# Kernel tuning notes

Measured on AMD Instinct MI355X. Metric: run time of the kernel, lower is better.

The kernel has to match this reference:

```python
import jax, jax.numpy as jnp
import numpy as np

B, N, DM, DE, H, L = 4, 256, 128, 8, 2 and 2, 8  # placeholder, real values below
B, N, DM, DE, H, L = 4, 256, 128, 8, 8, 2
D = DM // H  # per-head dim = 16
INNER = H * D


def setup_inputs() -> dict:
    key = jax.random.key(0)
    ks = jax.random.split(key, 20)
    nodes = jax.random.normal(ks[0], (B, N, DM), dtype=jnp.float32)
    edges = jax.random.normal(ks[1], (B, N, N, DE), dtype=jnp.float32)
    adjacency = (jax.random.uniform(ks[2], (B, N, N)) < 0.1).astype(jnp.float32)
    s = 0.02
    p = {
        'Wq': jax.random.normal(ks[3], (L, DM, INNER)) * s,
        'bq': jnp.zeros((L, INNER)),
        'Wk': jax.random.normal(ks[4], (L, DM, INNER)) * s,
        'bk': jnp.zeros((L, INNER)),
        'Wv': jax.random.normal(ks[5], (L, DM, INNER)) * s,
        'bv': jnp.zeros((L, INNER)),
        'We': jax.random.normal(ks[6], (L, DE, INNER)) * s,
        'be': jnp.zeros((L, INNER)),
        'Wres': jax.random.normal(ks[7], (L, DM, DM)) * s,
        'bres': jnp.zeros((L, DM)),
        'Wgate': jax.random.normal(ks[8], (L, 3 * DM, 1)) * s,
        'ln_g': jnp.ones((L, DM)),
        'ln_b': jnp.zeros((L, DM)),
    }
    return {'nodes': nodes, 'edges': edges, 'adjacency': adjacency, **p}


def _adj_softmax(sim, adj):
    # Faithful to source: torch.mean(x, dim, keepdim=True)[0] indexes batch 0,
    # giving a (N,1) shift broadcast over all batch*head rows.
    means = jnp.mean(sim, axis=-1, keepdims=True)[0]
    x_exp = jnp.exp(sim - means) * adj
    s = jnp.sum(x_exp, axis=-1, keepdims=True)
    s = jnp.where(s == 0, 1.0, s)
    return x_exp / s


def reference(nodes, edges, adjacency, Wq, bq, Wk, bk, Wv, bv, We, be,
              Wres, bres, Wgate, ln_g, ln_b):
    b, n, dm = nodes.shape
    h, d = H, DM // H
    scale = 1.0 / jnp.sqrt(jnp.float32(d))
    adj = jnp.broadcast_to(adjacency[:, None], (b, h, n, n)).reshape(b * h, n, n)
    x = nodes
    for l in range(L):  # fixed small layer count
        def heads(t):  # (b,n,h*d) -> (b*h, n, d)
            return t.reshape(b, n, h, d).transpose(0, 2, 1, 3).reshape(b * h, n, d)
        q = heads(x @ Wq[l] + bq[l])
        k = heads(x @ Wk[l] + bk[l])
        v = heads(x @ Wv[l] + bv[l])
        # edge features: (b,n,n,h,d) -> (b*h, n, n, d)
        e = (edges @ We[l] + be[l]).reshape(b, n, n, h, d)
        e = e.transpose(0, 3, 1, 2, 4).reshape(b * h, n, n, d)
        ke = k[:, None, :, :] + e
        ve = v[:, None, :, :] + e
        sim = jnp.einsum('bid,bijd->bij', q, ke) * scale
        attn = _adj_softmax(sim, adj)
        out = jnp.einsum('bij,bijd->bid', attn, ve)
        out = out.reshape(b, h, n, d).transpose(0, 2, 1, 3).reshape(b, n, h * d)
        # GatedResidual
        res = x @ Wres[l] + bres[l]
        gate_in = jnp.concatenate([out, res, out - res], axis=-1)
        g = jax.nn.sigmoid(gate_in @ Wgate[l])
        y = out * g + res * (1 - g)
        mu = jnp.mean(y, axis=-1, keepdims=True)
        var = jnp.var(y, axis=-1, keepdims=True)
        y = (y - mu) / jnp.sqrt(var + 1e-5) * ln_g[l] + ln_b[l]
        x = jax.nn.relu(y)
    return x
```

## Files before the change

### kernel.cpp

```cpp
#include <hip/hip_runtime.h>

#define BB 4
#define NN 256
#define DMM 128
#define DEE 8
#define HH 8
#define DD 16
#define LAYERS 2
#define SCALE 0.25f
#define PS 260
#define SS (BB*NN*DMM)


struct Params {
  const float *nodes, *edges, *adjacency;
  const float *Wq, *bq, *Wk, *bk, *Wv, *bv, *We, *be, *Wres, *bres, *Wgate, *lng, *lnb;
  const float *src;
  float *q, *k, *v, *res;
  float *out;
  int layer;
};

__global__ __launch_bounds__(256) void k_proj(Params P){
  const int t = threadIdx.x;
  const int m = t >> 6;
  const int cp = t & 63;
  const int row0 = blockIdx.x * 2;
  const int l = P.layer;
  const float *W, *bia; float* dst;
  if (m==0){ W = P.Wq + l*DMM*DMM; bia = P.bq + l*DMM; dst = P.q; }
  else if (m==1){ W = P.Wk + l*DMM*DMM; bia = P.bk + l*DMM; dst = P.k; }
  else if (m==2){ W = P.Wv + l*DMM*DMM; bia = P.bv + l*DMM; dst = P.v; }
  else { W = P.Wres + l*DMM*DMM; bia = P.bres + l*DMM; dst = P.res; }
  const float2 bv2 = *(const float2*)(bia + 2*cp);
  float a00=bv2.x, a01=bv2.y, a10=bv2.x, a11=bv2.y;
  const float2* W2 = (const float2*)W;
  const float* xr = P.src + (size_t)row0*DMM;
  #pragma unroll 8
  for (int kk=0; kk<DMM; kk++){
    float2 w = W2[kk*64+cp];
    float x0 = xr[kk], x1 = xr[DMM+kk];
    a00 += x0*w.x; a01 += x0*w.y;
    a10 += x1*w.x; a11 += x1*w.y;
  }
  if (m==1){
    const int b = row0 >> 8, i0 = row0 & 255;
    float* kT = dst + ((size_t)b*DMM + 2*cp)*NN;
    kT[i0]      = a00;  kT[NN + i0]     = a01;
    kT[i0+1]    = a10;  kT[NN + i0+1]   = a11;
  } else {
    *(float2*)(dst + (size_t)row0*DMM     + 2*cp) = make_float2(a00,a01);
    *(float2*)(dst + (size_t)(row0+1)*DMM + 2*cp) = make_float2(a10,a11);
  }
}

__global__ __launch_bounds__(512) void k_mid(Params P){
  const int t = threadIdx.x;
  const int r = t >> 8;
  const int u = t & 255;
  const int row0 = blockIdx.x*2;
  const int row  = row0 + r;
  const int b = row0 >> 8;

  __shared__ float xloc[2][128];
  __shared__ float qs[2][128];
  __shared__ float res_s[2][128];
  __shared__ float qwe_s[2][64];
  __shared__ float qbe_s[2][8];
  __shared__ float es[2][8*PS];
  __shared__ float ps[2][8*PS];
  __shared__ float red_s[2][32];
  __shared__ float ssum_s[2][8];
  __shared__ float g_s[2][64];
  __shared__ float red_a[2][2], red_b[2][2], red_c[2][2];

  if (u < 128) qs[r][u]        = P.q  [(size_t)row*DMM + u];
  else         res_s[r][u-128] = P.res[(size_t)row*DMM + (u-128)];
  const int j = u;
  float ec[8]; float adj;
  {
    const float4* er4 = (const float4*)(P.edges + ((size_t)row*NN + j)*DEE);
    float4 e0 = er4[0], e1 = er4[1];
    ec[0]=e0.x; ec[1]=e0.y; ec[2]=e0.z; ec[3]=e0.w;
    ec[4]=e1.x; ec[5]=e1.y; ec[6]=e1.z; ec[7]=e1.w;
    #pragma unroll
    for (int c=0;c<8;c++) es[r][c*PS+j] = ec[c];
    adj = P.adjacency[(size_t)row*NN + j];
  }
  __syncthreads();

  if (u < 64){
    const int h = u>>3, c = u&7;
    const float* Wer = P.We + c*DMM + h*DD;
    float a = 0.f;
    #pragma unroll
    for (int d=0; d<DD; d++) a += qs[r][h*DD+d]*Wer[d];
    qwe_s[r][u] = a;
    if (c==0){
      const float* ber = P.be + h*DD;
      float a2=0.f;
      #pragma unroll
      for (int d=0; d<DD; d++) a2 += qs[r][h*DD+d]*ber[d];
      qbe_s[r][h] = a2;
    }
  }
  __syncthreads();

  {
    const float* kTj = P.k + (size_t)b*DMM*NN + j;
    float preg[8];
    #pragma unroll
    for (int h=0; h<HH; h++){
      const float* kc = kTj + (size_t)(h*DD)*NN;
      float sim = qbe_s[r][h];
      #pragma unroll
      for (int d=0; d<DD; d++) sim += qs[r][h*DD+d] * kc[(size_t)d*NN];
      const float4* qw4 = (const float4*)(&qwe_s[r][h*8]);
      float4 wA=qw4[0], wB=qw4[1];
      sim += ec[0]*wA.x + ec[1]*wA.y + ec[2]*wA.z + ec[3]*wA.w;
      sim += ec[4]*wB.x + ec[5]*wB.y + ec[6]*wB.z + ec[7]*wB.w;
      sim *= SCALE;
      float p = __expf(sim)*adj;
      preg[h]=p; ps[r][h*PS+j]=p;
    }
    #pragma unroll
    for (int h=0; h<HH; h++){
      float v = preg[h];
      #pragma unroll
      for (int off=32; off; off>>=1) v += __shfl_xor(v, off, 64);
      if ((u&63)==0) red_s[r][(u>>6)*8+h] = v;
    }
  }
  __syncthreads();

  float pv = 0.f;
  if (u < 128){
    const int h = u>>4;
    const float* vcol = P.v + (size_t)b*NN*DMM + u;
    const float4* pr = (const float4*)(&ps[r][h*PS]);
    #pragma unroll 4
    for (int jq=0; jq<64; jq++){
      float4 pp = pr[jq];
      const float* vv = vcol + jq*4*DMM;
      pv += pp.x*vv[0] + pp.y*vv[DMM] + pp.z*vv[2*DMM] + pp.w*vv[3*DMM];
    }
  } else if (u < 192){
    const int h=(u-128)>>3, c=(u-128)&7;
    const float4* pr = (const float4*)(&ps[r][h*PS]);
    const float4* er = (const float4*)(&es[r][c*PS]);
    float g=0.f;
    #pragma unroll 4
    for (int jq=0; jq<64; jq++){
      float4 pp=pr[jq], ee=er[jq];
      g += pp.x*ee.x + pp.y*ee.y + pp.z*ee.z + pp.w*ee.w;
    }
    g_s[r][h*8+c]=g;
  } else if (u >= 248){
    const int h=u-248;
    ssum_s[r][h] = red_s[r][h]+red_s[r][8+h]+red_s[r][16+h]+red_s[r][24+h];
  }
  __syncthreads();

  float o=0.f, rr=0.f;
  if (u<128){
    const int h = u>>4;
    const float* Wec = P.We + u;
    float eacc=0.f;
    #pragma unroll
    for (int c=0;c<8;c++) eacc += Wec[c*DMM]*g_s[r][h*8+c];
    const float ssum = ssum_s[r][h];
    const float denom = (ssum==0.f)?1.f:ssum;
    const float bev = P.be[u];
    o = (pv + eacc + ssum*bev)/denom;
    rr = res_s[r][u];
    const float* Wg = P.Wgate;
    float contrib = o*Wg[u] + rr*Wg[DMM+u] + (o-rr)*Wg[2*DMM+u];
    #pragma unroll
    for (int off=32; off; off>>=1) contrib += __shfl_xor(contrib, off, 64);
    if ((u&63)==0) red_a[r][u>>6]=contrib;
  }
  __syncthreads();

  float y=0.f;
  if (u<128){
    const float gs = red_a[r][0]+red_a[r][1];
    const float gate = 1.f/(1.f+__expf(-gs));
    y = o*gate + rr*(1.f-gate);
    float s1=y, s2=y*y;
    #pragma unroll
    for (int off=32; off; off>>=1){ s1+=__shfl_xor(s1,off,64); s2+=__shfl_xor(s2,off,64); }
    if ((u&63)==0){ red_b[r][u>>6]=s1; red_c[r][u>>6]=s2; }
  }
  __syncthreads();

  if (u<128){
    const float mu  = (red_b[r][0]+red_b[r][1])*(1.f/128.f);
    const float var = (red_c[r][0]+red_c[r][1])*(1.f/128.f) - mu*mu;
    const float inv = rsqrtf(var+1e-5f);
    float yn = (y-mu)*inv*P.lng[u] + P.lnb[u];
    xloc[r][u] = fmaxf(yn, 0.f);
  }
  __syncthreads();

  {
    const int w = t>>6, m = w&3, ri = w>>2, cp = t&63;
    const float *W, *bia; float* dst;
    if (m==0){ W=P.Wq+DMM*DMM;   bia=P.bq+DMM;   dst=P.q;   }
    else if (m==1){ W=P.Wk+DMM*DMM;   bia=P.bk+DMM;   dst=P.k;   }
    else if (m==2){ W=P.Wv+DMM*DMM;   bia=P.bv+DMM;   dst=P.v;   }
    else          { W=P.Wres+DMM*DMM; bia=P.bres+DMM; dst=P.res; }
    const float2 bv2 = *(const float2*)(bia+2*cp);
    float a0=bv2.x, a1=bv2.y;
    const float2* W2 = (const float2*)W;
    const float* xr = xloc[ri];
    #pragma unroll 8
    for (int kk=0; kk<DMM; kk++){
      float2 w2 = W2[kk*64+cp];
      float xv = xr[kk];
      a0 += xv*w2.x; a1 += xv*w2.y;
    }
    const int prow = row0 + ri;
    if (m==1){
      const int pb = prow >> 8, pi = prow & 255;
      float* kT = dst + SS + ((size_t)pb*DMM + 2*cp)*NN;
      kT[pi] = a0; kT[NN + pi] = a1;
    } else {
      *(float2*)(dst + SS + (size_t)prow*DMM + 2*cp) = make_float2(a0,a1);
    }
  }
}

__global__ __launch_bounds__(256) void k_attn(Params P){
  const int t = threadIdx.x;
  const int b = blockIdx.x >> 8;
  const int i = blockIdx.x & 255;
  const int l = P.layer;

  __shared__ float qs[128];
  __shared__ float qwe_s[64];
  __shared__ float qbe_s[8];
  __shared__ float es[8*PS];
  __shared__ float ps[8*PS];
  __shared__ float red_s[32];
  __shared__ float ssum_s[8];
  __shared__ float g_s[64];
  __shared__ float res_s[128];
  __shared__ float red_a[2], red_b[2], red_c[2];

  if (t < 128) qs[t] = P.q[(b*NN+i)*DMM + t];
  __syncthreads();
  if (t < 64){
    const int h = t>>3, c = t&7;
    const float* Wer = P.We + l*DEE*DMM + c*DMM + h*DD;
    float a = 0.f;
    #pragma unroll
    for (int d=0; d<DD; d++) a += qs[h*DD+d]*Wer[d];
    qwe_s[t] = a;
    if (c==0){
      const float* ber = P.be + l*DMM + h*DD;
      float a2 = 0.f;
      #pragma unroll
      for (int d=0; d<DD; d++) a2 += qs[h*DD+d]*ber[d];
      qbe_s[h] = a2;
    }
  }
  __syncthreads();

  {
    const int j = t;
    const float4* er4 = (const float4*)(P.edges + ((size_t)(b*NN+i)*NN + j)*DEE);
    float4 e0 = er4[0], e1 = er4[1];
    float ec[8] = {e0.x,e0.y,e0.z,e0.w, e1.x,e1.y,e1.z,e1.w};
    #pragma unroll
    for (int c=0;c<8;c++) es[c*PS+j] = ec[c];
    const float adj = P.adjacency[(size_t)(b*NN+i)*NN + j];
    const float* kTj = P.k + (size_t)b*DMM*NN + j;
    float preg[8];
    #pragma unroll
    for (int h=0; h<HH; h++){
      const float* kc = kTj + (size_t)(h*DD)*NN;
      float sim = qbe_s[h];
      #pragma unroll
      for (int d=0; d<DD; d++) sim += qs[h*DD+d] * kc[(size_t)d*NN];
      const float4* qw4 = (const float4*)(qwe_s + h*8);
      float4 wA = qw4[0], wB = qw4[1];
      sim += ec[0]*wA.x + ec[1]*wA.y + ec[2]*wA.z + ec[3]*wA.w;
      sim += ec[4]*wB.x + ec[5]*wB.y + ec[6]*wB.z + ec[7]*wB.w;
      sim *= SCALE;
      float p = __expf(sim) * adj;
      preg[h] = p;
      ps[h*PS+j] = p;
    }
    #pragma unroll
    for (int h=0; h<HH; h++){
      float v = preg[h];
      #pragma unroll
      for (int off=32; off; off>>=1) v += __shfl_xor(v, off, 64);
      if ((t&63)==0) red_s[(t>>6)*8 + h] = v;
    }
  }
  __syncthreads();

  float pv = 0.f;
  if (t < 128){
    const int h = t>>4;
    const float* vcol = P.v + b*NN*DMM + t;
    const float4* pr = (const float4*)(ps + h*PS);
    #pragma unroll 4
    for (int jq=0; jq<64; jq++){
      float4 pp = pr[jq];
      const float* vv = vcol + jq*4*DMM;
      pv += pp.x*vv[0] + pp.y*vv[DMM] + pp.z*vv[2*DMM] + pp.w*vv[3*DMM];
    }
  } else if (t < 192){
    const int h = (t-128)>>3, c = (t-128)&7;
    const float4* pr = (const float4*)(ps + h*PS);
    const float4* er = (const float4*)(es + c*PS);
    float g = 0.f;
    #pragma unroll 4
    for (int jq=0; jq<64; jq++){
      float4 pp = pr[jq], ee = er[jq];
      g += pp.x*ee.x + pp.y*ee.y + pp.z*ee.z + pp.w*ee.w;
    }
    g_s[h*8+c] = g;
  } else {
    const int u = t - 192;
    const float2 rv = *(const float2*)(P.res + (b*NN+i)*DMM + 2*u);
    res_s[2*u] = rv.x; res_s[2*u+1] = rv.y;
    if (t >= 248){
      const int h = t - 248;
      ssum_s[h] = red_s[h] + red_s[8+h] + red_s[16+h] + red_s[24+h];
    }
  }
  __syncthreads();

  float o = 0.f, rr = 0.f;
  if (t < 128){
    const int h = t>>4;
    const float* Wec = P.We + l*DEE*DMM + t;
    float eacc = 0.f;
    #pragma unroll
    for (int c=0;c<8;c++) eacc += Wec[c*DMM] * g_s[h*8+c];
    const float ssum = ssum_s[h];
    const float denom = (ssum==0.f) ? 1.f : ssum;
    const float bev = P.be[l*DMM + t];
    o = (pv + eacc + ssum*bev) / denom;
    rr = res_s[t];
    const float* Wg = P.Wgate + l*3*DMM;
    float contrib = o*Wg[t] + rr*Wg[DMM+t] + (o-rr)*Wg[2*DMM+t];
    #pragma unroll
    for (int off=32; off; off>>=1) contrib += __shfl_xor(contrib, off, 64);
    if ((t&63)==0) red_a[t>>6] = contrib;
  }
  __syncthreads();

  float y = 0.f;
  if (t < 128){
    const float gs = red_a[0] + red_a[1];
    const float gate = 1.f/(1.f + __expf(-gs));
    y = o*gate + rr*(1.f-gate);
    float s1 = y, s2 = y*y;
    #pragma unroll
    for (int off=32; off; off>>=1){ s1 += __shfl_xor(s1, off, 64); s2 += __shfl_xor(s2, off, 64); }
    if ((t&63)==0){ red_b[t>>6] = s1; red_c[t>>6] = s2; }
  }
  __syncthreads();

  if (t < 128){
    const float mu  = (red_b[0]+red_b[1]) * (1.f/128.f);
    const float var = (red_c[0]+red_c[1]) * (1.f/128.f) - mu*mu;
    const float inv = rsqrtf(var + 1e-5f);
    float yn = (y - mu)*inv*P.lng[l*DMM+t] + P.lnb[l*DMM+t];
    yn = fmaxf(yn, 0.f);
    P.out[(b*NN+i)*DMM + t] = yn;
  }
}

extern "C" void kernel_launch(void* const* d_in, const int* in_sizes, int n_in,
                              void* d_out, int out_size, void* d_ws, size_t ws_size,
                              hipStream_t stream) {
  Params P;
  P.nodes     = (const float*)d_in[0];
  P.edges     = (const float*)d_in[1];
  P.adjacency = (const float*)d_in[2];
  P.Wq   = (const float*)d_in[3];  P.bq   = (const float*)d_in[4];
  P.Wk   = (const float*)d_in[5];  P.bk   = (const float*)d_in[6];
  P.Wv   = (const float*)d_in[7];  P.bv   = (const float*)d_in[8];
  P.We   = (const float*)d_in[9];  P.be   = (const float*)d_in[10];
  P.Wres = (const float*)d_in[11]; P.bres = (const float*)d_in[12];
  P.Wgate= (const float*)d_in[13];
  P.lng  = (const float*)d_in[14]; P.lnb  = (const float*)d_in[15];

  float* f = (float*)d_ws;
  float* qbuf = f;
  float* kbuf = f + 2*SS;
  float* vbuf = f + 4*SS;
  float* rbuf = f + 6*SS;
  P.out = (float*)d_out;

  P.layer = 0; P.src = P.nodes;
  P.q = qbuf; P.k = kbuf; P.v = vbuf; P.res = rbuf;
  hipLaunchKernelGGL(k_proj, dim3(BB*NN/2), dim3(256), 0, stream, P);

  hipLaunchKernelGGL(k_mid, dim3(BB*NN/2), dim3(512), 0, stream, P);

  P.layer = 1;
  P.q = qbuf + SS; P.k = kbuf + SS; P.v = vbuf + SS; P.res = rbuf + SS;
  hipLaunchKernelGGL(k_attn, dim3(BB*NN), dim3(256), 0, stream, P);
}
```

Measured before the change: 145.4 us.

## Remap attention score phase so each thread computes 4 keys for 2 heads

The score phase is reorganised in both k_mid and k_attn. Each thread now handles four consecutive key columns for two heads instead of one column for all eight heads. K, adjacency and edge data are read as float4, the q values are kept in registers, and each wave's shuffle reduction produces a per-head sum directly, which removes the red_s staging buffer and the cross-wave reduction step. In k_attn the edge tile load is also moved before the first barrier so it overlaps the q load. The trade-off is higher register pressure from holding 8 float4 K values and 16 q values per thread.

```diff
diff --git a/kernel.cpp b/kernel.cpp
--- a/kernel.cpp
+++ b/kernel.cpp
@@ -69,23 +69,18 @@
   __shared__ float qbe_s[2][8];
   __shared__ float es[2][8*PS];
   __shared__ float ps[2][8*PS];
-  __shared__ float red_s[2][32];
   __shared__ float ssum_s[2][8];
   __shared__ float g_s[2][64];
   __shared__ float red_a[2][2], red_b[2][2], red_c[2][2];
 
   if (u < 128) qs[r][u]        = P.q  [(size_t)row*DMM + u];
   else         res_s[r][u-128] = P.res[(size_t)row*DMM + (u-128)];
-  const int j = u;
-  float ec[8]; float adj;
   {
+    const int j = u;
     const float4* er4 = (const float4*)(P.edges + ((size_t)row*NN + j)*DEE);
     float4 e0 = er4[0], e1 = er4[1];
-    ec[0]=e0.x; ec[1]=e0.y; ec[2]=e0.z; ec[3]=e0.w;
-    ec[4]=e1.x; ec[5]=e1.y; ec[6]=e1.z; ec[7]=e1.w;
-    #pragma unroll
-    for (int c=0;c<8;c++) es[r][c*PS+j] = ec[c];
-    adj = P.adjacency[(size_t)row*NN + j];
+    es[r][0*PS+j]=e0.x; es[r][1*PS+j]=e0.y; es[r][2*PS+j]=e0.z; es[r][3*PS+j]=e0.w;
+    es[r][4*PS+j]=e1.x; es[r][5*PS+j]=e1.y; es[r][6*PS+j]=e1.z; es[r][7*PS+j]=e1.w;
   }
   __syncthreads();
 
@@ -107,29 +102,47 @@
   __syncthreads();
 
   {
-    const float* kTj = P.k + (size_t)b*DMM*NN + j;
-    float preg[8];
-    #pragma unroll
-    for (int h=0; h<HH; h++){
-      const float* kc = kTj + (size_t)(h*DD)*NN;
-      float sim = qbe_s[r][h];
-      #pragma unroll
-      for (int d=0; d<DD; d++) sim += qs[r][h*DD+d] * kc[(size_t)d*NN];
-      const float4* qw4 = (const float4*)(&qwe_s[r][h*8]);
-      float4 wA=qw4[0], wB=qw4[1];
-      sim += ec[0]*wA.x + ec[1]*wA.y + ec[2]*wA.z + ec[3]*wA.w;
-      sim += ec[4]*wB.x + ec[5]*wB.y + ec[6]*wB.z + ec[7]*wB.w;
-      sim *= SCALE;
-      float p = __expf(sim)*adj;
-      preg[h]=p; ps[r][h*PS+j]=p;
-    }
-    #pragma unroll
-    for (int h=0; h<HH; h++){
-      float v = preg[h];
-      #pragma unroll
-      for (int off=32; off; off>>=1) v += __shfl_xor(v, off, 64);
-      if ((u&63)==0) red_s[r][(u>>6)*8+h] = v;
-    }
+    const int dp = u>>6, jg = u&63;
+    const int J = 4*jg;
+    const float4 av = *(const float4*)(P.adjacency + (size_t)row*NN + J);
+    float hsum[2];
+    #pragma unroll
+    for (int hh=0; hh<2; hh++){
+      const int h = 2*dp+hh;
+      float qh[16];
+      #pragma unroll
+      for (int d=0; d<16; d++) qh[d] = qs[r][h*DD+d];
+      float s0=qbe_s[r][h]; float s1=s0, s2=s0, s3=s0;
+      const float* kbase = P.k + ((size_t)b*DMM + h*DD)*NN + J;
+      #pragma unroll
+      for (int db=0; db<2; db++){
+        float4 krg[8];
+        #pragma unroll
+        for (int d=0; d<8; d++) krg[d] = *(const float4*)(kbase + (size_t)(db*8+d)*NN);
+        #pragma unroll
+        for (int d=0; d<8; d++){
+          float qv = qh[db*8+d];
+          s0 += qv*krg[d].x; s1 += qv*krg[d].y; s2 += qv*krg[d].z; s3 += qv*krg[d].w;
+        }
+      }
+      #pragma unroll
+      for (int c=0; c<8; c++){
+        float4 ev = *(const float4*)(&es[r][c*PS + J]);
+        float wv = qwe_s[r][h*8+c];
+        s0 += wv*ev.x; s1 += wv*ev.y; s2 += wv*ev.z; s3 += wv*ev.w;
+      }
+      float4 p;
+      p.x = __expf(s0*SCALE)*av.x;
+      p.y = __expf(s1*SCALE)*av.y;
+      p.z = __expf(s2*SCALE)*av.z;
+      p.w = __expf(s3*SCALE)*av.w;
+      *(float4*)(&ps[r][h*PS + J]) = p;
+      hsum[hh] = (p.x+p.y)+(p.z+p.w);
+    }
+    float v0 = hsum[0], v1 = hsum[1];
+    #pragma unroll
+    for (int off=32; off; off>>=1){ v0 += __shfl_xor(v0,off,64); v1 += __shfl_xor(v1,off,64); }
+    if (jg==0){ ssum_s[r][2*dp] = v0; ssum_s[r][2*dp+1] = v1; }
   }
   __syncthreads();
 
@@ -155,9 +168,6 @@
       g += pp.x*ee.x + pp.y*ee.y + pp.z*ee.z + pp.w*ee.w;
     }
     g_s[r][h*8+c]=g;
-  } else if (u >= 248){
-    const int h=u-248;
-    ssum_s[r][h] = red_s[r][h]+red_s[r][8+h]+red_s[r][16+h]+red_s[r][24+h];
   }
   __syncthreads();
 
@@ -241,13 +251,19 @@
   __shared__ float qbe_s[8];
   __shared__ float es[8*PS];
   __shared__ float ps[8*PS];
-  __shared__ float red_s[32];
   __shared__ float ssum_s[8];
   __shared__ float g_s[64];
   __shared__ float res_s[128];
   __shared__ float red_a[2], red_b[2], red_c[2];
 
   if (t < 128) qs[t] = P.q[(b*NN+i)*DMM + t];
+  {
+    const int j = t;
+    const float4* er4 = (const float4*)(P.edges + ((size_t)(b*NN+i)*NN + j)*DEE);
+    float4 e0 = er4[0], e1 = er4[1];
+    es[0*PS+j]=e0.x; es[1*PS+j]=e0.y; es[2*PS+j]=e0.z; es[3*PS+j]=e0.w;
+    es[4*PS+j]=e1.x; es[5*PS+j]=e1.y; es[6*PS+j]=e1.z; es[7*PS+j]=e1.w;
+  }
   __syncthreads();
   if (t < 64){
     const int h = t>>3, c = t&7;
@@ -267,37 +283,47 @@
   __syncthreads();
 
   {
-    const int j = t;
-    const float4* er4 = (const float4*)(P.edges + ((size_t)(b*NN+i)*NN + j)*DEE);
-    float4 e0 = er4[0], e1 = er4[1];
-    float ec[8] = {e0.x,e0.y,e0.z,e0.w, e1.x,e1.y,e1.z,e1.w};
-    #pragma unroll
-    for (int c=0;c<8;c++) es[c*PS+j] = ec[c];
-    const float adj = P.adjacency[(size_t)(b*NN+i)*NN + j];
-    const float* kTj = P.k + (size_t)b*DMM*NN + j;
-    float preg[8];
-    #pragma unroll
-    for (int h=0; h<HH; h++){
-      const float* kc = kTj + (size_t)(h*DD)*NN;
-      float sim = qbe_s[h];
-      #pragma unroll
-      for (int d=0; d<DD; d++) sim += qs[h*DD+d] * kc[(size_t)d*NN];
-      const float4* qw4 = (const float4*)(qwe_s + h*8);
-      float4 wA = qw4[0], wB = qw4[1];
-      sim += ec[0]*wA.x + ec[1]*wA.y + ec[2]*wA.z + ec[3]*wA.w;
-      sim += ec[4]*wB.x + ec[5]*wB.y + ec[6]*wB.z + ec[7]*wB.w;
-      sim *= SCALE;
-      float p = __expf(sim) * adj;
-      preg[h] = p;
-      ps[h*PS+j] = p;
-    }
-    #pragma unroll
-    for (int h=0; h<HH; h++){
-      float v = preg[h];
-      #pragma unroll
-      for (int off=32; off; off>>=1) v += __shfl_xor(v, off, 64);
-      if ((t&63)==0) red_s[(t>>6)*8 + h] = v;
-    }
+    const int dp = t>>6, jg = t&63;
+    const int J = 4*jg;
+    const float4 av = *(const float4*)(P.adjacency + (size_t)(b*NN+i)*NN + J);
+    float hsum[2];
+    #pragma unroll
+    for (int hh=0; hh<2; hh++){
+      const int h = 2*dp+hh;
+      float qh[16];
+      #pragma unroll
+      for (int d=0; d<16; d++) qh[d] = qs[h*DD+d];
+      float s0=qbe_s[h]; float s1=s0, s2=s0, s3=s0;
+      const float* kbase = P.k + ((size_t)b*DMM + h*DD)*NN + J;
+      #pragma unroll
+      for (int db=0; db<2; db++){
+        float4 krg[8];
+        #pragma unroll
+        for (int d=0; d<8; d++) krg[d] = *(const float4*)(kbase + (size_t)(db*8+d)*NN);
+        #pragma unroll
+        for (int d=0; d<8; d++){
+          float qv = qh[db*8+d];
+          s0 += qv*krg[d].x; s1 += qv*krg[d].y; s2 += qv*krg[d].z; s3 += qv*krg[d].w;
+        }
+      }
+      #pragma unroll
+      for (int c=0; c<8; c++){
+        float4 ev = *(const float4*)(&es[c*PS + J]);
+        float wv = qwe_s[h*8+c];
+        s0 += wv*ev.x; s1 += wv*ev.y; s2 += wv*ev.z; s3 += wv*ev.w;
+      }
+      float4 p;
+      p.x = __expf(s0*SCALE)*av.x;
+      p.y = __expf(s1*SCALE)*av.y;
+      p.z = __expf(s2*SCALE)*av.z;
+      p.w = __expf(s3*SCALE)*av.w;
+      *(float4*)(&ps[h*PS + J]) = p;
+      hsum[hh] = (p.x+p.y)+(p.z+p.w);
+    }
+    float v0 = hsum[0], v1 = hsum[1];
+    #pragma unroll
+    for (int off=32; off; off>>=1){ v0 += __shfl_xor(v0,off,64); v1 += __shfl_xor(v1,off,64); }
+    if (jg==0){ ssum_s[2*dp] = v0; ssum_s[2*dp+1] = v1; }
   }
   __syncthreads();
 
@@ -327,10 +353,6 @@
     const int u = t - 192;
     const float2 rv = *(const float2*)(P.res + (b*NN+i)*DMM + 2*u);
     res_s[2*u] = rv.x; res_s[2*u+1] = rv.y;
-    if (t >= 248){
-      const int h = t - 248;
-      ssum_s[h] = red_s[h] + red_s[8+h] + red_s[16+h] + red_s[24+h];
-    }
   }
   __syncthreads();
 
```

New measurement: 146.8 us. No clear change (+1.0%).
